# Kernel optimization log

Measured on AMD Instinct MI355X. Metric: run time of the kernel, lower is better.

## Reference

```python
import jax, jax.numpy as jnp
import numpy as np

B, N, IN_DIM, OUT_DIM, K = 2, 8192, 64, 64, 16


def _mk_linear(key, out_d, in_d):
    k1, k2 = jax.random.split(key)
    W = jax.random.normal(k1, (out_d, in_d), dtype=jnp.float32) * 0.02
    b = jax.random.normal(k2, (out_d,), dtype=jnp.float32) * 0.02
    return W, b


def setup_inputs() -> dict:
    key = jax.random.key(0)
    ks = jax.random.split(key, 11)
    points_xyz = jax.random.normal(ks[0], (B, N, 3), dtype=jnp.float32)
    points_features = jax.random.normal(ks[1], (B, N, IN_DIM), dtype=jnp.float32)
    W1, b1 = _mk_linear(ks[2], OUT_DIM, IN_DIM)
    Wphi, bphi = _mk_linear(ks[3], OUT_DIM, OUT_DIM)
    Wpsi, bpsi = _mk_linear(ks[4], OUT_DIM, OUT_DIM)
    Walpha, balpha = _mk_linear(ks[5], OUT_DIM, OUT_DIM)
    Wgamma, bgamma = _mk_linear(ks[6], OUT_DIM, OUT_DIM)
    Wd1, bd1 = _mk_linear(ks[7], OUT_DIM, 3)
    Wd2, bd2 = _mk_linear(ks[8], OUT_DIM, OUT_DIM)
    W2, b2 = _mk_linear(ks[9], IN_DIM, OUT_DIM)
    return {
        "points_xyz": points_xyz, "points_features": points_features, "k": K,
        "W1": W1, "b1": b1, "Wphi": Wphi, "bphi": bphi, "Wpsi": Wpsi, "bpsi": bpsi,
        "Walpha": Walpha, "balpha": balpha, "Wgamma": Wgamma, "bgamma": bgamma,
        "Wd1": Wd1, "bd1": bd1, "Wd2": Wd2, "bd2": bd2, "W2": W2, "b2": b2,
    }


def _gather(points, idx):
    # points: [B, N, C], idx: [B, S, K] -> [B, S, K, C]
    return jax.vmap(lambda p, i: p[i])(points, idx)


def _knn_indices(xyz, k):
    # euclidean distances (as torch.cdist), then k smallest per query point
    sq = jnp.sum(xyz * xyz, axis=-1)  # [B, N]
    d2 = sq[:, :, None] + sq[:, None, :] - 2.0 * jnp.einsum('bnd,bmd->bnm', xyz, xyz)
    dist = jnp.sqrt(jnp.maximum(d2, 0.0))
    _, idx = jax.lax.top_k(-dist, k)  # smallest distances
    return idx  # [B, N, K]


def reference(points_xyz, points_features, k,
              W1, b1, Wphi, bphi, Wpsi, bpsi, Walpha, balpha, Wgamma, bgamma,
              Wd1, bd1, Wd2, bd2, W2, b2):
    idx = _knn_indices(points_xyz, k)                      # [B, N, K]
    neighbours_xyz = _gather(points_xyz, idx)              # [B, N, K, 3]

    f = points_features @ W1.T + b1                        # linear_1: [B, N, D]
    nf = _gather(f, idx)                                   # [B, N, K, D]

    # positional encoding: MLP on (p_i - p_j)
    diff = points_xyz[:, :, None, :] - neighbours_xyz      # [B, N, K, 3]
    delta = jax.nn.relu((diff @ Wd1.T + bd1) @ Wd2.T + bd2)  # [B, N, K, D]

    beta = (f @ Wphi.T + bphi)[:, :, None, :] - (nf @ Wpsi.T + bpsi) + delta
    gamma = beta @ Wgamma.T + bgamma
    rho = jax.nn.softmax(gamma, axis=-1)                   # softmax over channel dim (as in torch code)
    alpha = (nf @ Walpha.T + balpha) + delta
    out = jnp.sum(rho * alpha, axis=2)                     # reduce over K -> [B, N, D]

    out = out @ W2.T + b2 + points_features                # linear_2 + residual
    return (points_xyz, out)
```

## Files before the change

### kernel.cpp

```cpp
#include <hip/hip_runtime.h>

#define NB 2
#define NP 8192
#define D 64
#define KNN 16
#define NBK 256

__global__ void __launch_bounds__(256)
k_foldall(const float* __restrict__ Wg,   const float* __restrict__ bg,
          const float* __restrict__ Wphi, const float* __restrict__ bphi,
          const float* __restrict__ Wpsi, const float* __restrict__ bpsi,
          const float* __restrict__ Wal,  const float* __restrict__ bal,
          const float* __restrict__ W1,   const float* __restrict__ b1,
          const float* __restrict__ Wd1,  const float* __restrict__ bd1,
          const float* __restrict__ Wd2,  const float* __restrict__ bd2,
          float* __restrict__ Af, float* __restrict__ dAv,
          float* __restrict__ Bf, float* __restrict__ dBv,
          float* __restrict__ Cf, float* __restrict__ dCv,
          float* __restrict__ comb)
{
  __shared__ float sT[64 * 65];
  __shared__ float sTb[64];
  __shared__ float4 sWeff[64];
  const int m   = blockIdx.x;
  const int tid = threadIdx.x;

  if (m == 3) {
    if (tid < 64) {
      const int c = tid;
      float wx = 0.f, wy = 0.f, wz = 0.f, be = bd2[c];
      for (int k = 0; k < 64; ++k) {
        float w = Wd2[c*64 + k];
        wx = fmaf(w, Wd1[k*3+0], wx);
        wy = fmaf(w, Wd1[k*3+1], wy);
        wz = fmaf(w, Wd1[k*3+2], wz);
        be = fmaf(w, bd1[k], be);
      }
      sWeff[c] = make_float4(wx, wy, wz, be);
    }
    __syncthreads();
    #pragma unroll
    for (int it = 0; it < 16; ++it) {
      const int e = it*256 + tid;
      const int o = e >> 6, c = e & 63;
      comb[c*68 + 4 + o] = Wg[e];
    }
    if (tid < 64) {
      float4 wf = sWeff[tid];
      comb[tid*68+0] = wf.x; comb[tid*68+1] = wf.y;
      comb[tid*68+2] = wf.z; comb[tid*68+3] = wf.w;
    }
    return;
  }

  const int o = tid >> 2;
  const int q = tid & 3;

  const float* O  = (m == 2) ? Wal : Wg;
  const float* M  = (m == 0) ? Wphi : Wpsi;
  const float* bM = (m == 0) ? bphi : bpsi;

  if (m == 2) {
    for (int cc = 0; cc < 16; ++cc) sT[o*65 + q*16 + cc] = Wal[o*64 + q*16 + cc];
    if (q == 0) sTb[o] = bal[o];
  } else {
    float acc[16];
    #pragma unroll
    for (int cc = 0; cc < 16; ++cc) acc[cc] = 0.f;
    for (int k = 0; k < 64; ++k) {
      float w = O[o*64 + k];
      #pragma unroll
      for (int cc = 0; cc < 16; ++cc) acc[cc] = fmaf(w, M[k*64 + q*16 + cc], acc[cc]);
    }
    for (int cc = 0; cc < 16; ++cc) sT[o*65 + q*16 + cc] = acc[cc];
    if (q == 0) {
      float tb = (m == 0) ? bg[o] : 0.f;
      for (int k = 0; k < 64; ++k) tb = fmaf(O[o*64 + k], bM[k], tb);
      sTb[o] = tb;
    }
  }
  __syncthreads();

  float acc[16];
  #pragma unroll
  for (int cc = 0; cc < 16; ++cc) acc[cc] = 0.f;
  for (int k = 0; k < 64; ++k) {
    float w = sT[o*65 + k];
    #pragma unroll
    for (int cc = 0; cc < 16; ++cc) acc[cc] = fmaf(w, W1[k*64 + q*16 + cc], acc[cc]);
  }
  float* R  = (m == 0) ? Af  : (m == 1) ? Bf  : Cf;
  float* dR = (m == 0) ? dAv : (m == 1) ? dBv : dCv;
  for (int cc = 0; cc < 16; ++cc) R[o*64 + q*16 + cc] = acc[cc];
  if (q == 0) {
    float db = sTb[o];
    for (int k = 0; k < 64; ++k) db = fmaf(sT[o*65 + k], b1[k], db);
    dR[o] = db;
  }
}

__global__ void __launch_bounds__(256)
k_buckets(const float* __restrict__ xyz, float4* __restrict__ brange,
          int* __restrict__ bcur)
{
  __shared__ float smn[256], smx[256];
  __shared__ int hcnt[NBK];
  __shared__ float sr[2];
  const int b = blockIdx.x, tid = threadIdx.x;

  float mn = 1e30f, mx = -1e30f;
  for (int i = tid; i < NP; i += 256) {
    float x = xyz[((size_t)b * NP + i) * 3];
    mn = fminf(mn, x); mx = fmaxf(mx, x);
  }
  smn[tid] = mn; smx[tid] = mx; __syncthreads();
  for (int off = 128; off >= 1; off >>= 1) {
    if (tid < off) {
      smn[tid] = fminf(smn[tid], smn[tid+off]);
      smx[tid] = fmaxf(smx[tid], smx[tid+off]);
    }
    __syncthreads();
  }
  if (tid == 0) {
    float xmin = smn[0], xmax = smx[0];
    float wdt = fmaxf((xmax - xmin) / (float)NBK, 1e-20f);
    brange[b] = make_float4(xmin, 1.0f / wdt, wdt, 0.f);
    sr[0] = xmin; sr[1] = 1.0f / wdt;
  }
  hcnt[tid] = 0;
  __syncthreads();

  const float xmin = sr[0], inv = sr[1];
  for (int i = tid; i < NP; i += 256) {
    float x = xyz[((size_t)b * NP + i) * 3];
    int k = min(max((int)((x - xmin) * inv), 0), NBK - 1);
    atomicAdd(&hcnt[k], 1);
  }
  __syncthreads();

  int v = hcnt[tid];
  int acc = v;
  for (int off = 1; off < NBK; off <<= 1) {
    int t = (tid >= off) ? hcnt[tid - off] : 0;
    __syncthreads();
    acc += t; hcnt[tid] = acc;
    __syncthreads();
  }
  bcur[b*NBK + tid] = acc - v;
}

__global__ void __launch_bounds__(256)
k_scatter(const float* __restrict__ xyz, const float4* __restrict__ brange,
          int* __restrict__ bcur, float4* __restrict__ spts, int* __restrict__ ssidx,
          int* __restrict__ rank)
{
  const int i = blockIdx.x * 256 + threadIdx.x;
  const int b = i >> 13;
  const int orig = i & (NP - 1);
  const float x = xyz[(size_t)i*3+0];
  const float y = xyz[(size_t)i*3+1];
  const float z = xyz[(size_t)i*3+2];
  const float sq = __fadd_rn(__fadd_rn(__fmul_rn(x,x), __fmul_rn(y,y)), __fmul_rn(z,z));
  float4 br = brange[b];
  int k = min(max((int)((x - br.x) * br.y), 0), NBK - 1);
  int pos = atomicAdd(&bcur[b*NBK + k], 1);
  spts [(size_t)b * NP + pos] = make_float4(x, y, z, sq);
  ssidx[(size_t)b * NP + pos] = orig;
  rank [(size_t)b * NP + orig] = pos;
}

__global__ void __launch_bounds__(256, 2)
k_transform4(const float* __restrict__ feat, const int* __restrict__ ssidx,
             const float* __restrict__ Af, const float* __restrict__ dAv,
             const float* __restrict__ Bf, const float* __restrict__ dBv,
             const float* __restrict__ Cf, const float* __restrict__ dCv,
             float* __restrict__ uA, float* __restrict__ uB, float* __restrict__ uC)
{
  const int tid   = threadIdx.x;
  const int chunk = blockIdx.y;
  const int m     = chunk >> 2;
  const int rb    = (chunk & 3) << 4;
  const float* __restrict__ M  = (m == 0) ? Af  : ((m == 1) ? Bf  : Cf);
  const float* __restrict__ dv = (m == 0) ? dAv : ((m == 1) ? dBv : dCv);
  float* __restrict__ O        = (m == 0) ? uA  : ((m == 1) ? uB  : uC);

  const size_t p = (size_t)blockIdx.x * 256 + tid;
  const int b = (int)(p >> 13);
  const int orig = ssidx[p];
  const size_t frow = ((size_t)(b << 13) + orig) * D;

  const float4* xr = (const float4*)(feat + frow);
  float x[64];
  #pragma unroll
  for (int c4 = 0; c4 < 16; ++c4) {
    float4 v = xr[c4];
    x[c4*4+0] = v.x; x[c4*4+1] = v.y; x[c4*4+2] = v.z; x[c4*4+3] = v.w;
  }

  float acc[16];
  #pragma unroll
  for (int r = 0; r < 16; ++r) {
    acc[r] = dv[rb + r];
    const float4* wr = (const float4*)(M + (size_t)(rb + r) * D);
    #pragma unroll
    for (int c4 = 0; c4 < 16; ++c4) {
      float4 w = wr[c4];
      acc[r] = fmaf(w.x, x[c4*4+0], acc[r]);
      acc[r] = fmaf(w.y, x[c4*4+1], acc[r]);
      acc[r] = fmaf(w.z, x[c4*4+2], acc[r]);
      acc[r] = fmaf(w.w, x[c4*4+3], acc[r]);
    }
  }
  float4* op = (float4*)(O + p * D + rb);
  #pragma unroll
  for (int q = 0; q < 4; ++q)
    op[q] = make_float4(acc[q*4+0], acc[q*4+1], acc[q*4+2], acc[q*4+3]);
}

__global__ void __launch_bounds__(256)
k_knn8(const float4* __restrict__ spts, const int* __restrict__ ssidx,
       const float4* __restrict__ brange, int* __restrict__ knn_idx)
{
  const int qpos = (blockIdx.x * 256 + threadIdx.x) >> 6;
  const int lane = threadIdx.x & 63;
  const int b    = qpos >> 13;
  const int pos  = qpos & (NP - 1);
  const size_t bb = (size_t)b * NP;

  const float4 qp = spts[bb + pos];
  const float xi = qp.x, yi = qp.y, zi = qp.z, sqi = qp.w;
  const int si_q = ssidx[bb + pos];

  const float slack = __fmul_rn(brange[b].z, 1.01f);

  const int p0 = min(max(pos - 32, 0), NP - 64);

  unsigned kds, kidx;
  float thr_d2;

#define THR_REFRESH()                                                                    \
  {                                                                                      \
    float d16 = __uint_as_float((unsigned)__builtin_amdgcn_readlane((int)kds, KNN - 1)); \
    thr_d2 = __fmul_rn(__fmul_rn(d16, d16), 1.000001f);                                  \
  }

#define KPROCS(P, SIV, VALID)                                                            \
  {                                                                                      \
    float dot = __fadd_rn(__fadd_rn(__fmul_rn(xi,(P).x), __fmul_rn(yi,(P).y)),           \
                          __fmul_rn(zi,(P).z));                                          \
    float d2  = __fsub_rn(__fadd_rn(sqi, (P).w), __fmul_rn(2.0f, dot));                  \
    unsigned long long mask = __ballot((VALID) && d2 <= thr_d2);                         \
    if (mask) {                                                                          \
      float ds = __fsqrt_rn(fmaxf(d2, 0.0f));                                            \
      unsigned cds = __float_as_uint(ds);                                                \
      unsigned cidx = (unsigned)(SIV);                                                   \
      bool ins = false;                                                                  \
      do {                                                                               \
        const int src = __ffsll((long long)mask) - 1;                                    \
        mask &= mask - 1;                                                                \
        const unsigned ids  = (unsigned)__builtin_amdgcn_readlane((int)cds,  src);       \
        const unsigned iidx = (unsigned)__builtin_amdgcn_readlane((int)cidx, src);       \
        const bool less = (kds < ids) || ((kds == ids) && (kidx < iidx));                \
        const int pos2 = __popcll(__ballot((lane < KNN) && less));                       \
        if (pos2 < KNN) {                                                                \
          unsigned uds  = __shfl_up(kds,  1, 64);                                        \
          unsigned uidx = __shfl_up(kidx, 1, 64);                                        \
          if (lane < KNN) {                                                              \
            kds  = (lane < pos2) ? kds  : (lane == pos2 ? ids  : uds);                   \
            kidx = (lane < pos2) ? kidx : (lane == pos2 ? iidx : uidx);                  \
          }                                                                              \
          ins = true;                                                                    \
        }                                                                                \
      } while (mask);                                                                    \
      if (ins) THR_REFRESH()                                                             \
    }                                                                                    \
  }

  {
    float4 P = spts[bb + p0 + lane];
    int SI = ssidx[bb + p0 + lane];
    float dot = __fadd_rn(__fadd_rn(__fmul_rn(xi,P.x), __fmul_rn(yi,P.y)), __fmul_rn(zi,P.z));
    float d2  = __fsub_rn(__fadd_rn(sqi, P.w), __fmul_rn(2.0f, dot));
    float ds  = __fsqrt_rn(fmaxf(d2, 0.0f));
    kds  = __float_as_uint(ds);
    kidx = (unsigned)SI;
  }
  #pragma unroll
  for (int k = 2; k <= 64; k <<= 1) {
    #pragma unroll
    for (int jj = k >> 1; jj >= 1; jj >>= 1) {
      unsigned ods  = __shfl_xor(kds,  jj, 64);
      unsigned oidx = __shfl_xor(kidx, jj, 64);
      const bool up    = (lane & k) == 0;
      const bool lower = (lane & jj) == 0;
      const bool takemin = (lower == up);
      const bool oless = (ods < kds) || ((ods == kds) && (oidx < kidx));
      const bool take = (takemin == oless);
      kds  = take ? ods  : kds;
      kidx = take ? oidx : kidx;
    }
  }
  if (lane >= KNN) { kds = 0x7F7FFFFFu; kidx = 0xFFFFu; }
  THR_REFRESH()

  int l = p0 - 1;
  int r = p0 + 64;
  bool goL = (l >= 0), goR = (r < NP);
  #pragma unroll 1
  while (goL || goR) {
    if (goL) {
      float xl = spts[bb + l].x;
      float gap = (xi - xl) - slack;
      if (gap > 0.f && __fmul_rn(gap, gap) > thr_d2 + 1e-3f) {
        goL = false;
      } else {
        const int base = max(l - 63, 0);
        const int cl = base + lane;
        const bool valid = cl <= l;
        float4 P = spts[bb + cl];
        int SI = ssidx[bb + cl];
        KPROCS(P, SI, valid)
        l = base - 1;
        goL = (l >= 0);
      }
    }
    if (goR) {
      float xr = spts[bb + r].x;
      float gap = (xr - xi) - slack;
      if (gap > 0.f && __fmul_rn(gap, gap) > thr_d2 + 1e-3f) {
        goR = false;
      } else {
        const int cl = min(r + lane, NP - 1);
        const bool valid = (r + lane) < NP;
        float4 P = spts[bb + cl];
        int SI = ssidx[bb + cl];
        KPROCS(P, SI, valid)
        r += 64;
        goR = (r < NP);
      }
    }
  }
#undef KPROCS
#undef THR_REFRESH

  if (lane < KNN) knn_idx[((size_t)b * NP + si_q) * KNN + lane] = (int)kidx;
}

__global__ void __launch_bounds__(256, 4)
k_main7(const float4* __restrict__ spts, const int* __restrict__ ssidx,
        const int* __restrict__ rank,
        const float* __restrict__ feat,
        const int* __restrict__ knn_idx,
        const float* __restrict__ uA, const float* __restrict__ uB, const float* __restrict__ uC,
        const float* __restrict__ comb,
        const float* __restrict__ W2g, const float* __restrict__ b2g,
        float* __restrict__ out)
{
  __shared__ float sW2[64 * 68];
  __shared__ float sB2[64];
  __shared__ float sY[16 * 68];

  const int tid = threadIdx.x;
  {
    #pragma unroll
    for (int it = 0; it < 16; ++it) {
      const int e = it*256 + tid;
      sW2[(e >> 6)*68 + (e & 63)] = W2g[e];
    }
    if (tid < 64) sB2[tid] = b2g[tid];
  }
  __syncthreads();

  const int lane  = tid & 63;
  const int kslot = lane & 15;
  const int plocal = (tid >> 6) * 4 + (lane >> 4);
  const int p_s   = blockIdx.x * 16 + plocal;
  const int b     = p_s >> 13;
  const size_t bb = (size_t)b * NP;

  const int orig_i = ssidx[p_s];
  const size_t orow = (bb + (size_t)orig_i) * D;
  const size_t irow = (size_t)p_s * D;

  const int j = knn_idx[(bb + (size_t)orig_i) * KNN + kslot];
  const int jpos = rank[bb + (size_t)j];
  const size_t jrow = (bb + (size_t)jpos) * D;

  const float4 pi = spts[p_s];
  const float4 pj = spts[bb + (size_t)jpos];
  const float dx = pi.x - pj.x;
  const float dy = pi.y - pj.y;
  const float dz = pi.z - pj.z;

  float gamma[64];
  {
    const float4* ua = (const float4*)(uA + irow);
    const float4* ub = (const float4*)(uB + jrow);
    #pragma unroll
    for (int cc = 0; cc < 16; ++cc) {
      float4 a = ua[cc];
      float4 v = ub[cc];
      gamma[cc*4+0] = a.x - v.x; gamma[cc*4+1] = a.y - v.y;
      gamma[cc*4+2] = a.z - v.z; gamma[cc*4+3] = a.w - v.w;
    }
  }

  #pragma unroll 4
  for (int c = 0; c < 64; ++c) {
    const float4* rec = (const float4*)(comb + c*68);
    float4 wf = rec[0];
    float t = fmaf(wf.z, dz, fmaf(wf.y, dy, fmaf(wf.x, dx, wf.w)));
    float d = fmaxf(t, 0.f);
    #pragma unroll
    for (int o4 = 0; o4 < 16; ++o4) {
      float4 w = rec[1 + o4];
      gamma[o4*4+0] = fmaf(w.x, d, gamma[o4*4+0]);
      gamma[o4*4+1] = fmaf(w.y, d, gamma[o4*4+1]);
      gamma[o4*4+2] = fmaf(w.z, d, gamma[o4*4+2]);
      gamma[o4*4+3] = fmaf(w.w, d, gamma[o4*4+3]);
    }
  }

  float m0 = gamma[0], m1 = gamma[1], m2 = gamma[2], m3 = gamma[3];
  #pragma unroll
  for (int c = 4; c < 64; c += 4) {
    m0 = fmaxf(m0, gamma[c+0]); m1 = fmaxf(m1, gamma[c+1]);
    m2 = fmaxf(m2, gamma[c+2]); m3 = fmaxf(m3, gamma[c+3]);
  }
  const float m = fmaxf(fmaxf(m0, m1), fmaxf(m2, m3));
  float s0 = 0.f, s1 = 0.f, s2 = 0.f, s3 = 0.f;
  #pragma unroll
  for (int c = 0; c < 64; c += 4) {
    gamma[c+0] = __expf(gamma[c+0] - m); s0 += gamma[c+0];
    gamma[c+1] = __expf(gamma[c+1] - m); s1 += gamma[c+1];
    gamma[c+2] = __expf(gamma[c+2] - m); s2 += gamma[c+2];
    gamma[c+3] = __expf(gamma[c+3] - m); s3 += gamma[c+3];
  }
  const float inv = 1.0f / ((s0 + s1) + (s2 + s3));

  {
    const float4* uc = (const float4*)(uC + jrow);
    #pragma unroll
    for (int cc = 0; cc < 16; ++cc) {
      float4 av = uc[cc];
      float avv[4] = {av.x, av.y, av.z, av.w};
      #pragma unroll
      for (int r = 0; r < 4; ++r) {
        const int c = cc*4 + r;
        const float4* rec = (const float4*)(comb + c*68);
        float4 wf = rec[0];
        float t = fmaf(wf.z, dz, fmaf(wf.y, dy, fmaf(wf.x, dx, wf.w)));
        float d = fmaxf(t, 0.f);
        gamma[c] = gamma[c] * inv * (avv[r] + d);
      }
    }
  }

  float t8[32];
  {
    const bool hi = (kslot & 8) != 0;
    #pragma unroll
    for (int i2 = 0; i2 < 32; ++i2) {
      float sendv = hi ? gamma[i2] : gamma[i2+32];
      float keepv = hi ? gamma[i2+32] : gamma[i2];
      t8[i2] = keepv + __shfl_xor(sendv, 8, 64);
    }
  }
  float t4[16];
  {
    const bool hi = (kslot & 4) != 0;
    #pragma unroll
    for (int i2 = 0; i2 < 16; ++i2) {
      float sendv = hi ? t8[i2] : t8[i2+16];
      float keepv = hi ? t8[i2+16] : t8[i2];
      t4[i2] = keepv + __shfl_xor(sendv, 4, 64);
    }
  }
  float t2[8];
  {
    const bool hi = (kslot & 2) != 0;
    #pragma unroll
    for (int i2 = 0; i2 < 8; ++i2) {
      float sendv = hi ? t4[i2] : t4[i2+8];
      float keepv = hi ? t4[i2+8] : t4[i2];
      t2[i2] = keepv + __shfl_xor(sendv, 2, 64);
    }
  }
  float y0, y1, y2, y3;
  {
    const bool hi = (kslot & 1) != 0;
    float s0v = hi ? t2[0] : t2[4];
    float s1v = hi ? t2[1] : t2[5];
    float s2v = hi ? t2[2] : t2[6];
    float s3v = hi ? t2[3] : t2[7];
    float k0 = hi ? t2[4] : t2[0];
    float k1 = hi ? t2[5] : t2[1];
    float k2 = hi ? t2[6] : t2[2];
    float k3 = hi ? t2[7] : t2[3];
    y0 = k0 + __shfl_xor(s0v, 1, 64);
    y1 = k1 + __shfl_xor(s1v, 1, 64);
    y2 = k2 + __shfl_xor(s2v, 1, 64);
    y3 = k3 + __shfl_xor(s3v, 1, 64);
  }

  ((float4*)sY)[plocal * 17 + kslot] = make_float4(y0, y1, y2, y3);
  __syncthreads();
  float y[64];
  {
    const float4* yp = (const float4*)sY + plocal * 17;
    #pragma unroll
    for (int o4 = 0; o4 < 16; ++o4) {
      float4 v = yp[o4];
      y[o4*4+0] = v.x; y[o4*4+1] = v.y; y[o4*4+2] = v.z; y[o4*4+3] = v.w;
    }
  }

  const int oc = kslot * 4;
  float o0 = sB2[oc+0], o1 = sB2[oc+1], o2 = sB2[oc+2], o3 = sB2[oc+3];
  {
    const float4* r0 = (const float4*)(sW2 + (oc+0)*68);
    const float4* r1 = (const float4*)(sW2 + (oc+1)*68);
    const float4* r2 = (const float4*)(sW2 + (oc+2)*68);
    const float4* r3 = (const float4*)(sW2 + (oc+3)*68);
    #pragma unroll
    for (int c4 = 0; c4 < 16; ++c4) {
      float4 w0 = r0[c4], w1 = r1[c4], w2 = r2[c4], w3 = r3[c4];
      o0 = fmaf(w0.x, y[c4*4+0], o0); o0 = fmaf(w0.y, y[c4*4+1], o0);
      o0 = fmaf(w0.z, y[c4*4+2], o0); o0 = fmaf(w0.w, y[c4*4+3], o0);
      o1 = fmaf(w1.x, y[c4*4+0], o1); o1 = fmaf(w1.y, y[c4*4+1], o1);
      o1 = fmaf(w1.z, y[c4*4+2], o1); o1 = fmaf(w1.w, y[c4*4+3], o1);
      o2 = fmaf(w2.x, y[c4*4+0], o2); o2 = fmaf(w2.y, y[c4*4+1], o2);
      o2 = fmaf(w2.z, y[c4*4+2], o2); o2 = fmaf(w2.w, y[c4*4+3], o2);
      o3 = fmaf(w3.x, y[c4*4+0], o3); o3 = fmaf(w3.y, y[c4*4+1], o3);
      o3 = fmaf(w3.z, y[c4*4+2], o3); o3 = fmaf(w3.w, y[c4*4+3], o3);
    }
  }
  float4 fv = ((const float4*)(feat + orow))[kslot];
  ((float4*)(out + orow))[kslot] = make_float4(o0 + fv.x, o1 + fv.y, o2 + fv.z, o3 + fv.w);
}

extern "C" void kernel_launch(void* const* d_in, const int* in_sizes, int n_in,
                              void* d_out, int out_size, void* d_ws, size_t ws_size,
                              hipStream_t stream) {
  const float* xyz  = (const float*)d_in[0];
  const float* feat = (const float*)d_in[1];
  const float* W1   = (const float*)d_in[3];
  const float* b1   = (const float*)d_in[4];
  const float* Wphi = (const float*)d_in[5];
  const float* bphi = (const float*)d_in[6];
  const float* Wpsi = (const float*)d_in[7];
  const float* bpsi = (const float*)d_in[8];
  const float* Wal  = (const float*)d_in[9];
  const float* bal  = (const float*)d_in[10];
  const float* Wg   = (const float*)d_in[11];
  const float* bg   = (const float*)d_in[12];
  const float* Wd1  = (const float*)d_in[13];
  const float* bd1  = (const float*)d_in[14];
  const float* Wd2  = (const float*)d_in[15];
  const float* bd2  = (const float*)d_in[16];
  const float* W2   = (const float*)d_in[17];
  const float* b2   = (const float*)d_in[18];

  float* out = (float*)d_out;

  const size_t NPT = (size_t)NB * NP;
  float* uA = (float*)d_ws;
  float* uB = uA + NPT * D;
  float* uC = uB + NPT * D;
  int* knn_idx = (int*)(uC + NPT * D);
  float* Af  = (float*)(knn_idx + NPT * KNN);
  float* dAv = Af + 4096;
  float* Bf  = dAv + 64;
  float* dBv = Bf + 4096;
  float* Cf  = dBv + 64;
  float* dCv = Cf + 4096;
  float* comb = dCv + 64;
  int* bcur   = (int*)(comb + 64*68);
  float4* brange = (float4*)(bcur + NB*NBK);
  float4* spts   = brange + 4;
  int* ssidx     = (int*)(spts + NPT);
  int* rank      = ssidx + NPT;

  hipMemcpyAsync(d_out, d_in[0], NPT * 3 * sizeof(float),
                 hipMemcpyDeviceToDevice, stream);

  k_foldall<<<4, 256, 0, stream>>>(Wg, bg, Wphi, bphi, Wpsi, bpsi, Wal, bal, W1, b1,
                                   Wd1, bd1, Wd2, bd2,
                                   Af, dAv, Bf, dBv, Cf, dCv, comb);
  k_buckets<<<NB, 256, 0, stream>>>(xyz, brange, bcur);
  k_scatter<<<NPT / 256, 256, 0, stream>>>(xyz, brange, bcur, spts, ssidx, rank);
  k_transform4<<<dim3(64, 12), 256, 0, stream>>>(feat, ssidx, Af, dAv, Bf, dBv, Cf, dCv,
                                                 uA, uB, uC);
  k_knn8<<<NPT / 4, 256, 0, stream>>>(spts, ssidx, brange, knn_idx);
  k_main7<<<NPT / 16, 256, 0, stream>>>(spts, ssidx, rank, feat, knn_idx,
                                        uA, uB, uC, comb, W2, b2, out + NPT * 3);
}
```

Baseline: 223.2 us.

## Merge independent kernels and prefetch next KNN candidate chunks

Merges the weight-folding and bucket-histogram kernels into one launch, and merges the feature-transform kernel into the KNN kernel as extra blocks so both run concurrently. In the KNN scan loop, the next left and right 64-point chunks are prefetched before the current ones are processed. The boundary x-coordinate is read with readlane instead of a separate global load. The changes aim to cut launch gaps and hide load latency in the serial scan, at the cost of higher register pressure and a mixed-workload kernel whose launch bounds no longer suit the transform path (its min-blocks hint of 2 is dropped).

```diff
diff --git a/kernel.cpp b/kernel.cpp
--- a/kernel.cpp
+++ b/kernel.cpp
@@ -5,25 +5,79 @@
 #define D 64
 #define KNN 16
 #define NBK 256
+#define KNN_BLOCKS (NB * NP / 4)
+
+__device__ __forceinline__ float rl_f(float v, int lane) {
+  return __uint_as_float((unsigned)__builtin_amdgcn_readlane((int)__float_as_uint(v), lane));
+}
 
 __global__ void __launch_bounds__(256)
-k_foldall(const float* __restrict__ Wg,   const float* __restrict__ bg,
-          const float* __restrict__ Wphi, const float* __restrict__ bphi,
-          const float* __restrict__ Wpsi, const float* __restrict__ bpsi,
-          const float* __restrict__ Wal,  const float* __restrict__ bal,
-          const float* __restrict__ W1,   const float* __restrict__ b1,
-          const float* __restrict__ Wd1,  const float* __restrict__ bd1,
-          const float* __restrict__ Wd2,  const float* __restrict__ bd2,
-          float* __restrict__ Af, float* __restrict__ dAv,
-          float* __restrict__ Bf, float* __restrict__ dBv,
-          float* __restrict__ Cf, float* __restrict__ dCv,
-          float* __restrict__ comb)
+k_foldbuckets(const float* __restrict__ Wg,   const float* __restrict__ bg,
+              const float* __restrict__ Wphi, const float* __restrict__ bphi,
+              const float* __restrict__ Wpsi, const float* __restrict__ bpsi,
+              const float* __restrict__ Wal,  const float* __restrict__ bal,
+              const float* __restrict__ W1,   const float* __restrict__ b1,
+              const float* __restrict__ Wd1,  const float* __restrict__ bd1,
+              const float* __restrict__ Wd2,  const float* __restrict__ bd2,
+              const float* __restrict__ xyz,
+              float* __restrict__ Af, float* __restrict__ dAv,
+              float* __restrict__ Bf, float* __restrict__ dBv,
+              float* __restrict__ Cf, float* __restrict__ dCv,
+              float* __restrict__ comb,
+              float4* __restrict__ brange, int* __restrict__ bcur)
 {
   __shared__ float sT[64 * 65];
   __shared__ float sTb[64];
   __shared__ float4 sWeff[64];
+  __shared__ float smn[256], smx[256];
+  __shared__ int hcnt[NBK];
+  __shared__ float sr[2];
   const int m   = blockIdx.x;
   const int tid = threadIdx.x;
+
+  if (m >= 4) {
+    const int b = m - 4;
+    float mn = 1e30f, mx = -1e30f;
+    for (int i = tid; i < NP; i += 256) {
+      float x = xyz[((size_t)b * NP + i) * 3];
+      mn = fminf(mn, x); mx = fmaxf(mx, x);
+    }
+    smn[tid] = mn; smx[tid] = mx; __syncthreads();
+    for (int off = 128; off >= 1; off >>= 1) {
+      if (tid < off) {
+        smn[tid] = fminf(smn[tid], smn[tid+off]);
+        smx[tid] = fmaxf(smx[tid], smx[tid+off]);
+      }
+      __syncthreads();
+    }
+    if (tid == 0) {
+      float xmin = smn[0], xmax = smx[0];
+      float wdt = fmaxf((xmax - xmin) / (float)NBK, 1e-20f);
+      brange[b] = make_float4(xmin, 1.0f / wdt, wdt, 0.f);
+      sr[0] = xmin; sr[1] = 1.0f / wdt;
+    }
+    hcnt[tid] = 0;
+    __syncthreads();
+
+    const float xmin = sr[0], inv = sr[1];
+    for (int i = tid; i < NP; i += 256) {
+      float x = xyz[((size_t)b * NP + i) * 3];
+      int k = min(max((int)((x - xmin) * inv), 0), NBK - 1);
+      atomicAdd(&hcnt[k], 1);
+    }
+    __syncthreads();
+
+    int v = hcnt[tid];
+    int acc = v;
+    for (int off = 1; off < NBK; off <<= 1) {
+      int t = (tid >= off) ? hcnt[tid - off] : 0;
+      __syncthreads();
+      acc += t; hcnt[tid] = acc;
+      __syncthreads();
+    }
+    bcur[b*NBK + tid] = acc - v;
+    return;
+  }
 
   if (m == 3) {
     if (tid < 64) {
@@ -97,56 +151,6 @@
     for (int k = 0; k < 64; ++k) db = fmaf(sT[o*65 + k], b1[k], db);
     dR[o] = db;
   }
-}
-
-__global__ void __launch_bounds__(256)
-k_buckets(const float* __restrict__ xyz, float4* __restrict__ brange,
-          int* __restrict__ bcur)
-{
-  __shared__ float smn[256], smx[256];
-  __shared__ int hcnt[NBK];
-  __shared__ float sr[2];
-  const int b = blockIdx.x, tid = threadIdx.x;
-
-  float mn = 1e30f, mx = -1e30f;
-  for (int i = tid; i < NP; i += 256) {
-    float x = xyz[((size_t)b * NP + i) * 3];
-    mn = fminf(mn, x); mx = fmaxf(mx, x);
-  }
-  smn[tid] = mn; smx[tid] = mx; __syncthreads();
-  for (int off = 128; off >= 1; off >>= 1) {
-    if (tid < off) {
-      smn[tid] = fminf(smn[tid], smn[tid+off]);
-      smx[tid] = fmaxf(smx[tid], smx[tid+off]);
-    }
-    __syncthreads();
-  }
-  if (tid == 0) {
-    float xmin = smn[0], xmax = smx[0];
-    float wdt = fmaxf((xmax - xmin) / (float)NBK, 1e-20f);
-    brange[b] = make_float4(xmin, 1.0f / wdt, wdt, 0.f);
-    sr[0] = xmin; sr[1] = 1.0f / wdt;
-  }
-  hcnt[tid] = 0;
-  __syncthreads();
-
-  const float xmin = sr[0], inv = sr[1];
-  for (int i = tid; i < NP; i += 256) {
-    float x = xyz[((size_t)b * NP + i) * 3];
-    int k = min(max((int)((x - xmin) * inv), 0), NBK - 1);
-    atomicAdd(&hcnt[k], 1);
-  }
-  __syncthreads();
-
-  int v = hcnt[tid];
-  int acc = v;
-  for (int off = 1; off < NBK; off <<= 1) {
-    int t = (tid >= off) ? hcnt[tid - off] : 0;
-    __syncthreads();
-    acc += t; hcnt[tid] = acc;
-    __syncthreads();
-  }
-  bcur[b*NBK + tid] = acc - v;
 }
 
 __global__ void __launch_bounds__(256)
@@ -169,60 +173,63 @@
   rank [(size_t)b * NP + orig] = pos;
 }
 
-__global__ void __launch_bounds__(256, 2)
-k_transform4(const float* __restrict__ feat, const int* __restrict__ ssidx,
-             const float* __restrict__ Af, const float* __restrict__ dAv,
-             const float* __restrict__ Bf, const float* __restrict__ dBv,
-             const float* __restrict__ Cf, const float* __restrict__ dCv,
-             float* __restrict__ uA, float* __restrict__ uB, float* __restrict__ uC)
+__global__ void __launch_bounds__(256)
+k_knn_tf(const float4* __restrict__ spts, const int* __restrict__ ssidx,
+         const float4* __restrict__ brange, int* __restrict__ knn_idx,
+         const float* __restrict__ feat,
+         const float* __restrict__ Af, const float* __restrict__ dAv,
+         const float* __restrict__ Bf, const float* __restrict__ dBv,
+         const float* __restrict__ Cf, const float* __restrict__ dCv,
+         float* __restrict__ uA, float* __restrict__ uB, float* __restrict__ uC)
 {
-  const int tid   = threadIdx.x;
-  const int chunk = blockIdx.y;
-  const int m     = chunk >> 2;
-  const int rb    = (chunk & 3) << 4;
-  const float* __restrict__ M  = (m == 0) ? Af  : ((m == 1) ? Bf  : Cf);
-  const float* __restrict__ dv = (m == 0) ? dAv : ((m == 1) ? dBv : dCv);
-  float* __restrict__ O        = (m == 0) ? uA  : ((m == 1) ? uB  : uC);
-
-  const size_t p = (size_t)blockIdx.x * 256 + tid;
-  const int b = (int)(p >> 13);
-  const int orig = ssidx[p];
-  const size_t frow = ((size_t)(b << 13) + orig) * D;
-
-  const float4* xr = (const float4*)(feat + frow);
-  float x[64];
-  #pragma unroll
-  for (int c4 = 0; c4 < 16; ++c4) {
-    float4 v = xr[c4];
-    x[c4*4+0] = v.x; x[c4*4+1] = v.y; x[c4*4+2] = v.z; x[c4*4+3] = v.w;
-  }
-
-  float acc[16];
-  #pragma unroll
-  for (int r = 0; r < 16; ++r) {
-    acc[r] = dv[rb + r];
-    const float4* wr = (const float4*)(M + (size_t)(rb + r) * D);
+  const int tid = threadIdx.x;
+
+  if (blockIdx.x >= KNN_BLOCKS) {
+    const int tb    = blockIdx.x - KNN_BLOCKS;
+    const int chunk = tb >> 6;
+    const int xblk  = tb & 63;
+    const int m     = chunk >> 2;
+    const int rb    = (chunk & 3) << 4;
+    const float* __restrict__ M  = (m == 0) ? Af  : ((m == 1) ? Bf  : Cf);
+    const float* __restrict__ dv = (m == 0) ? dAv : ((m == 1) ? dBv : dCv);
+    float* __restrict__ O        = (m == 0) ? uA  : ((m == 1) ? uB  : uC);
+
+    const size_t p = (size_t)xblk * 256 + tid;
+    const int b = (int)(p >> 13);
+    const int orig = ssidx[p];
+    const size_t frow = ((size_t)(b << 13) + orig) * D;
+
+    const float4* xr = (const float4*)(feat + frow);
+    float x[64];
     #pragma unroll
     for (int c4 = 0; c4 < 16; ++c4) {
-      float4 w = wr[c4];
-      acc[r] = fmaf(w.x, x[c4*4+0], acc[r]);
-      acc[r] = fmaf(w.y, x[c4*4+1], acc[r]);
-      acc[r] = fmaf(w.z, x[c4*4+2], acc[r]);
-      acc[r] = fmaf(w.w, x[c4*4+3], acc[r]);
-    }
-  }
-  float4* op = (float4*)(O + p * D + rb);
-  #pragma unroll
-  for (int q = 0; q < 4; ++q)
-    op[q] = make_float4(acc[q*4+0], acc[q*4+1], acc[q*4+2], acc[q*4+3]);
-}
-
-__global__ void __launch_bounds__(256)
-k_knn8(const float4* __restrict__ spts, const int* __restrict__ ssidx,
-       const float4* __restrict__ brange, int* __restrict__ knn_idx)
-{
-  const int qpos = (blockIdx.x * 256 + threadIdx.x) >> 6;
-  const int lane = threadIdx.x & 63;
+      float4 v = xr[c4];
+      x[c4*4+0] = v.x; x[c4*4+1] = v.y; x[c4*4+2] = v.z; x[c4*4+3] = v.w;
+    }
+
+    float acc[16];
+    #pragma unroll
+    for (int r = 0; r < 16; ++r) {
+      acc[r] = dv[rb + r];
+      const float4* wr = (const float4*)(M + (size_t)(rb + r) * D);
+      #pragma unroll
+      for (int c4 = 0; c4 < 16; ++c4) {
+        float4 w = wr[c4];
+        acc[r] = fmaf(w.x, x[c4*4+0], acc[r]);
+        acc[r] = fmaf(w.y, x[c4*4+1], acc[r]);
+        acc[r] = fmaf(w.z, x[c4*4+2], acc[r]);
+        acc[r] = fmaf(w.w, x[c4*4+3], acc[r]);
+      }
+    }
+    float4* op = (float4*)(O + p * D + rb);
+    #pragma unroll
+    for (int q = 0; q < 4; ++q)
+      op[q] = make_float4(acc[q*4+0], acc[q*4+1], acc[q*4+2], acc[q*4+3]);
+    return;
+  }
+
+  const int qpos = (blockIdx.x * 256 + tid) >> 6;
+  const int lane = tid & 63;
   const int b    = qpos >> 13;
   const int pos  = qpos & (NP - 1);
   const size_t bb = (size_t)b * NP;
@@ -306,36 +313,46 @@
   int l = p0 - 1;
   int r = p0 + 64;
   bool goL = (l >= 0), goR = (r < NP);
+  int baseL = max(l - 63, 0);
+
+  float4 PL, PR; int SL = 0, SR = 0;
+  if (goL) { PL = spts[bb + baseL + lane]; SL = ssidx[bb + baseL + lane]; }
+  if (goR) { const int cl = min(r + lane, NP - 1); PR = spts[bb + cl]; SR = ssidx[bb + cl]; }
+
   #pragma unroll 1
   while (goL || goR) {
+    const int nl = baseL - 1;
+    const int nbaseL = max(nl - 63, 0);
+    const int nr = r + 64;
+    const bool hasNL = goL && (nl >= 0);
+    const bool hasNR = goR && (nr < NP);
+    float4 nPL, nPR; int nSL = 0, nSR = 0;
+    if (hasNL) { nPL = spts[bb + nbaseL + lane]; nSL = ssidx[bb + nbaseL + lane]; }
+    if (hasNR) { const int cl = min(nr + lane, NP - 1); nPR = spts[bb + cl]; nSR = ssidx[bb + cl]; }
+
     if (goL) {
-      float xl = spts[bb + l].x;
-      float gap = (xi - xl) - slack;
+      const float xl = rl_f(PL.x, l - baseL);
+      const float gap = (xi - xl) - slack;
       if (gap > 0.f && __fmul_rn(gap, gap) > thr_d2 + 1e-3f) {
         goL = false;
       } else {
-        const int base = max(l - 63, 0);
-        const int cl = base + lane;
-        const bool valid = cl <= l;
-        float4 P = spts[bb + cl];
-        int SI = ssidx[bb + cl];
-        KPROCS(P, SI, valid)
-        l = base - 1;
+        const bool valid = (baseL + lane) <= l;
+        KPROCS(PL, SL, valid)
+        l = nl; baseL = nbaseL;
+        PL = nPL; SL = nSL;
         goL = (l >= 0);
       }
     }
     if (goR) {
-      float xr = spts[bb + r].x;
-      float gap = (xr - xi) - slack;
+      const float xr = rl_f(PR.x, 0);
+      const float gap = (xr - xi) - slack;
       if (gap > 0.f && __fmul_rn(gap, gap) > thr_d2 + 1e-3f) {
         goR = false;
       } else {
-        const int cl = min(r + lane, NP - 1);
         const bool valid = (r + lane) < NP;
-        float4 P = spts[bb + cl];
-        int SI = ssidx[bb + cl];
-        KPROCS(P, SI, valid)
-        r += 64;
+        KPROCS(PR, SR, valid)
+        r = nr;
+        PR = nPR; SR = nSR;
         goR = (r < NP);
       }
     }
@@ -584,14 +601,13 @@
   hipMemcpyAsync(d_out, d_in[0], NPT * 3 * sizeof(float),
                  hipMemcpyDeviceToDevice, stream);
 
-  k_foldall<<<4, 256, 0, stream>>>(Wg, bg, Wphi, bphi, Wpsi, bpsi, Wal, bal, W1, b1,
-                                   Wd1, bd1, Wd2, bd2,
-                                   Af, dAv, Bf, dBv, Cf, dCv, comb);
-  k_buckets<<<NB, 256, 0, stream>>>(xyz, brange, bcur);
+  k_foldbuckets<<<6, 256, 0, stream>>>(Wg, bg, Wphi, bphi, Wpsi, bpsi, Wal, bal, W1, b1,
+                                       Wd1, bd1, Wd2, bd2, xyz,
+                                       Af, dAv, Bf, dBv, Cf, dCv, comb, brange, bcur);
   k_scatter<<<NPT / 256, 256, 0, stream>>>(xyz, brange, bcur, spts, ssidx, rank);
-  k_transform4<<<dim3(64, 12), 256, 0, stream>>>(feat, ssidx, Af, dAv, Bf, dBv, Cf, dCv,
+  k_knn_tf<<<KNN_BLOCKS + 768, 256, 0, stream>>>(spts, ssidx, brange, knn_idx,
+                                                 feat, Af, dAv, Bf, dBv, Cf, dCv,
                                                  uA, uB, uC);
-  k_knn8<<<NPT / 4, 256, 0, stream>>>(spts, ssidx, brange, knn_idx);
   k_main7<<<NPT / 16, 256, 0, stream>>>(spts, ssidx, rank, feat, knn_idx,
                                         uA, uB, uC, comb, W2, b2, out + NPT * 3);
 }
```

Measured after the change: 196.0 us. -12.2%, faster.
